# Optimization experiments

Measured on AMD Instinct MI355X. Metric: run time of the kernel, lower is better.

The kernel has to match this reference:

```python
import jax, jax.numpy as jnp
import numpy as np

L, N, EMB, H = 4, 50000, 128, 4
R, HID, LBL = 16, 64, 32
E = 625000


def setup_inputs() -> dict:
    key = jax.random.key(0)
    ks = jax.random.split(key, 10)
    s = 0.05
    return {
        "embedding": jax.random.normal(ks[0], (L, N, EMB), jnp.float32),
        "in_proj_w": jax.random.normal(ks[1], (3 * EMB, EMB), jnp.float32) * s,
        "in_proj_b": jnp.zeros((3 * EMB,), jnp.float32),
        "out_proj_w": jax.random.normal(ks[2], (EMB, EMB), jnp.float32) * s,
        "out_proj_b": jnp.zeros((EMB,), jnp.float32),
        "w1": jax.random.normal(ks[3], (R, EMB, HID), jnp.float32) * s,
        "root1": jax.random.normal(ks[4], (EMB, HID), jnp.float32) * s,
        "b1": jnp.zeros((HID,), jnp.float32),
        "w2": jax.random.normal(ks[5], (R, HID, LBL), jnp.float32) * s,
        "root2": jax.random.normal(ks[6], (HID, LBL), jnp.float32) * s,
        "b2": jnp.zeros((LBL,), jnp.float32),
        "edge_index": jax.random.randint(ks[7], (2, E), 0, N, dtype=jnp.int64),
        "edge_type": jax.random.randint(ks[8], (E,), 0, R, dtype=jnp.int64),
    }


def mha_self(x, wi, bi, wo, bo):
    # x: (L, N, EMB) -- torch nn.MultiheadAttention, batch_first=False, q=k=v=x
    Ls, Ns, Es = x.shape
    hd = Es // H
    qkv = x @ wi.T + bi                      # (L, N, 3E)
    q, k, v = jnp.split(qkv, 3, axis=-1)
    q = q.reshape(Ls, Ns, H, hd)
    k = k.reshape(Ls, Ns, H, hd)
    v = v.reshape(Ls, Ns, H, hd)
    scores = jnp.einsum('lnhd,mnhd->nhlm', q, k) / np.sqrt(hd).astype(np.float32)
    attn = jax.nn.softmax(scores, axis=-1)
    out = jnp.einsum('nhlm,mnhd->lnhd', attn, v).reshape(Ls, Ns, Es)
    return out @ wo.T + bo


def rgcn_layer(x, src, dst, etype, W, root, bias):
    # PyG RGCNConv (num_bases=None, aggr='mean'):
    # out[n] = x[n] @ root + bias + sum_r mean_{e: dst=n, type=r} x[src_e] @ W[r]
    Rr, fin, fout = W.shape
    seg = etype * N + dst                                   # (E,) combined (rel, dst)
    msg_sum = jax.ops.segment_sum(x[src], seg, num_segments=Rr * N)   # (R*N, fin)
    cnt = jax.ops.segment_sum(jnp.ones((src.shape[0],), x.dtype), seg,
                              num_segments=Rr * N)
    mean = (msg_sum / jnp.maximum(cnt, 1.0)[:, None]).reshape(Rr, N, fin)
    agg = jnp.einsum('rni,rio->no', mean, W)                # per-relation GEMM
    return agg + x @ root + bias


def reference(embedding, in_proj_w, in_proj_b, out_proj_w, out_proj_b,
              w1, root1, b1, w2, root2, b2, edge_index, edge_type):
    attn_out = mha_self(embedding, in_proj_w, in_proj_b, out_proj_w, out_proj_b)
    x = attn_out[0]                                         # (N, EMB)
    src, dst = edge_index[0], edge_index[1]
    x = jax.nn.relu(rgcn_layer(x, src, dst, edge_type, w1, root1, b1))
    x = rgcn_layer(x, src, dst, edge_type, w2, root2, b2)
    return jax.nn.softmax(x, axis=-1)
```

## Files before the change

kernel.cpp:

```cpp
#include <hip/hip_runtime.h>
#include <hip/hip_bf16.h>
#include <math.h>

#define NNODES 50000
#define NEDGE 625000
#define RREL 16
#define SCAN_NB 196

typedef __attribute__((ext_vector_type(8))) short short8;
typedef __attribute__((ext_vector_type(4))) float f32x4;

__device__ __forceinline__ float bfu(ushort u) {
  return __uint_as_float(((unsigned)u) << 16);
}
__device__ __forceinline__ ushort f2b(float f) {
  __hip_bfloat16 h = __float2bfloat16(f);
  return *(ushort*)&h;
}

__global__ __launch_bounds__(256) void mega_prep(
    const float* __restrict__ ipw, const float* __restrict__ opw,
    const float* __restrict__ w1, const float* __restrict__ root1,
    const float* __restrict__ w2, const float* __restrict__ root2,
    const float* __restrict__ opb,
    const int* __restrict__ dst, const int* __restrict__ et,
    __hip_bfloat16* __restrict__ BTqkv, __hip_bfloat16* __restrict__ BToutT,
    __hip_bfloat16* __restrict__ BT1, __hip_bfloat16* __restrict__ BT2,
    float* __restrict__ bias1, int* __restrict__ cnt) {
  int b = blockIdx.x, t = threadIdx.x;
  if (b < 944) {
    int i = b * 256 + t;
    if (i < 49152) {
      BTqkv[i] = __float2bfloat16(ipw[i]);
    } else if (i < 65536) {
      int j = i - 49152; int m = j / 128, c = j % 128;
      BToutT[j] = __float2bfloat16(opw[c * 128 + m]);
    } else if (i < 65536 + 139264) {
      int j = i - 65536; int c = j / 128, k = j % 128;
      float v;
      if (c < 64) v = root1[k * 64 + c];
      else { int r = (c - 64) >> 6, o = (c - 64) & 63; v = w1[r * 8192 + k * 64 + o]; }
      BT1[j] = __float2bfloat16(v);
    } else if (i < 65536 + 139264 + 34816) {
      int j = i - 65536 - 139264; int c = j / 64, k = j % 64;
      float v;
      if (c < 32) v = root2[k * 32 + c];
      else { int r = (c - 32) >> 5, o = (c - 32) & 31; v = w2[r * 2048 + k * 32 + o]; }
      BT2[j] = __float2bfloat16(v);
    }
  } else if (b < 949) {
    int j = (b - 944) * 256 + t;
    if (j < 1088) {
      float s = 0.f;
      if (j < 64) {
        for (int c = 0; c < 128; c++) s += opb[c] * root1[c * 64 + j];
      } else {
        int r = (j - 64) >> 6, o = (j - 64) & 63;
        for (int c = 0; c < 128; c++) s += opb[c] * w1[r * 8192 + c * 64 + o];
      }
      bias1[j] = s;
    }
  } else {
    int e = (b - 949) * 256 + t;
    if (e < NEDGE) atomicAdd(&cnt[et[e] * NNODES + dst[e]], 1);
  }
}

__global__ __launch_bounds__(256) void qkv_gemm(
    const float* __restrict__ A, const __hip_bfloat16* __restrict__ BT,
    const float* __restrict__ bias, __hip_bfloat16* __restrict__ C) {
  __shared__ ushort As[128 * 128];
  __shared__ ushort Cs[128 * 136];
  const int t = threadIdx.x;
  const long row0 = (long)blockIdx.x * 128;

  {
    float4 fa[16];
#pragma unroll
    for (int it = 0; it < 8; it++) {
      int c = t + it * 256;
      int r = c >> 4, cc = c & 15;
      long gm = row0 + r; if (gm > 199999) gm = 199999;
      const float* ap = A + gm * 128 + cc * 8;
      fa[2 * it]     = *(const float4*)ap;
      fa[2 * it + 1] = *(const float4*)(ap + 4);
    }
#pragma unroll
    for (int it = 0; it < 8; it++) {
      int c = t + it * 256;
      int r = c >> 4, cc = c & 15;
      int4 v = make_int4(0, 0, 0, 0);
      if (row0 + r < 200000) {
        float4 f0 = fa[2 * it], f1 = fa[2 * it + 1];
        v.x = (int)f2b(f0.x) | ((int)f2b(f0.y) << 16);
        v.y = (int)f2b(f0.z) | ((int)f2b(f0.w) << 16);
        v.z = (int)f2b(f1.x) | ((int)f2b(f1.y) << 16);
        v.w = (int)f2b(f1.z) | ((int)f2b(f1.w) << 16);
      }
      *(int4*)(As + r * 128 + ((cc ^ (r & 7)) * 8)) = v;
    }
  }
  __syncthreads();

  const int lane = t & 63, w = t >> 6;
  const int wr = (w >> 1) * 64, wc = (w & 1) * 64;
  const int lrow = lane & 15, lk = lane >> 4;
  const int nstrips = (row0 < NNODES) ? 3 : 2;

  for (int s = 0; s < nstrips; s++) {
    const int col0 = (s == 2) ? 0 : 128 + s * 128;
    const long Meff = (s == 2) ? NNODES : 200000;

    const ushort* bp[4];
#pragma unroll
    for (int j = 0; j < 4; j++)
      bp[j] = (const ushort*)BT + (long)(col0 + wc + j * 16 + lrow) * 128 + lk * 8;

    short8 bfr[4][4];
#pragma unroll
    for (int k0 = 0; k0 < 4; k0++)
#pragma unroll
      for (int j = 0; j < 4; j++)
        bfr[k0][j] = *(const short8*)(bp[j] + k0 * 32);

    f32x4 acc[4][4];
#pragma unroll
    for (int i = 0; i < 4; i++)
#pragma unroll
      for (int j = 0; j < 4; j++) acc[i][j] = (f32x4){0.f, 0.f, 0.f, 0.f};

#pragma unroll
    for (int k0 = 0; k0 < 4; k0++) {
      const int cb = k0 * 4 + lk;
      short8 af[4];
#pragma unroll
      for (int i = 0; i < 4; i++) {
        int ra = wr + i * 16 + lrow;
        af[i] = *(const short8*)(As + ra * 128 + ((cb ^ (ra & 7)) * 8));
      }
#pragma unroll
      for (int i = 0; i < 4; i++)
#pragma unroll
        for (int j = 0; j < 4; j++)
          acc[i][j] = __builtin_amdgcn_mfma_f32_16x16x32_bf16(af[i], bfr[k0][j], acc[i][j], 0, 0, 0);
    }

    __syncthreads();
#pragma unroll
    for (int j = 0; j < 4; j++) {
      int coll = wc + j * 16 + lrow;
      float bv = bias[col0 + coll];
#pragma unroll
      for (int i = 0; i < 4; i++) {
        int rbase = wr + i * 16 + lk * 4;
#pragma unroll
        for (int q = 0; q < 4; q++)
          Cs[(rbase + q) * 136 + coll] = f2b(acc[i][j][q] + bv);
      }
    }
    __syncthreads();
#pragma unroll
    for (int idx = t; idx < 128 * 16; idx += 256) {
      int r = idx >> 4, k = idx & 15;
      long gm = row0 + r;
      if (gm < Meff)
        *(int4*)((ushort*)C + gm * 384 + col0 + k * 8) = *(const int4*)(Cs + r * 136 + k * 8);
    }
  }
}

#define EPILOGUE_STORE(MEFF, NCOLS, LDC, BIASEXPR)                              \
  for (int p = 0; p < 2; p++) {                                                 \
    __syncthreads();                                                            \
    if ((w >> 1) == p) {                                                        \
      _Pragma("unroll")                                                         \
      for (int j = 0; j < 4; j++) {                                             \
        int coll = wc + j * 16 + lrow;                                          \
        float bv = (BIASEXPR);                                                  \
        _Pragma("unroll")                                                       \
        for (int i = 0; i < 4; i++) {                                           \
          int rloc = i * 16 + lk * 4;                                           \
          _Pragma("unroll")                                                     \
          for (int q = 0; q < 4; q++)                                           \
            Cs[(rloc + q) * 132 + coll] = f2b(acc[i][j][q] + bv);               \
        }                                                                       \
      }                                                                         \
    }                                                                           \
    __syncthreads();                                                            \
    _Pragma("unroll")                                                           \
    for (int idx = t; idx < 64 * 16; idx += 256) {                              \
      int r = idx >> 4, k = idx & 15;                                           \
      long gm = row0 + p * 64 + r;                                              \
      int col = col0 + k * 8;                                                   \
      if (gm < (MEFF) && col < (NCOLS))                                         \
        *(int4*)((ushort*)C + gm * (LDC) + col) = *(const int4*)(Cs + r * 132 + k * 8); \
    }                                                                           \
  }

template <int K>
__global__ __launch_bounds__(256) void gemm_strips(
    const __hip_bfloat16* __restrict__ Av, const __hip_bfloat16* __restrict__ BT,
    const float* __restrict__ bias, __hip_bfloat16* __restrict__ C,
    int M, int N, int ldc, int spg) {
  constexpr int CPR = K / 8;
  constexpr int NIT = 128 * CPR / 256;
  constexpr int NK0 = K / 32;
  __shared__ ushort As[128 * K];
  __shared__ ushort Cs[64 * 132];
  const int t = threadIdx.x;
  const long row0 = (long)blockIdx.x * 128;

  {
    int4 st[NIT];
#pragma unroll
    for (int it = 0; it < NIT; it++) {
      int c = t + it * 256;
      int r = c / CPR, cc = c % CPR;
      long gm = row0 + r; if (gm > M - 1) gm = M - 1;
      st[it] = *(const int4*)((const ushort*)Av + gm * K + cc * 8);
    }
#pragma unroll
    for (int it = 0; it < NIT; it++) {
      int c = t + it * 256;
      int r = c / CPR, cc = c % CPR;
      int4 v = (row0 + r < M) ? st[it] : make_int4(0, 0, 0, 0);
      *(int4*)(As + r * K + ((cc ^ (r & 7)) * 8)) = v;
    }
  }
  __syncthreads();

  const int lane = t & 63, w = t >> 6;
  const int wr = (w >> 1) * 64, wc = (w & 1) * 64;
  const int lrow = lane & 15, lk = lane >> 4;
  const int nstrips = (N + 127) / 128;
  const int sbeg = blockIdx.y * spg;
  const int send = min(sbeg + spg, nstrips);

  for (int s = sbeg; s < send; s++) {
    const int col0 = s * 128;

    const ushort* bp[4];
#pragma unroll
    for (int j = 0; j < 4; j++) {
      int gn = col0 + wc + j * 16 + lrow;
      if (gn > N - 1) gn = N - 1;
      bp[j] = (const ushort*)BT + (long)gn * K + lk * 8;
    }

    short8 bfr[NK0][4];
#pragma unroll
    for (int k0 = 0; k0 < NK0; k0++)
#pragma unroll
      for (int j = 0; j < 4; j++)
        bfr[k0][j] = *(const short8*)(bp[j] + k0 * 32);

    f32x4 acc[4][4];
#pragma unroll
    for (int i = 0; i < 4; i++)
#pragma unroll
      for (int j = 0; j < 4; j++) acc[i][j] = (f32x4){0.f, 0.f, 0.f, 0.f};

#pragma unroll
    for (int k0 = 0; k0 < NK0; k0++) {
      const int cb = k0 * 4 + lk;
      short8 af[4];
#pragma unroll
      for (int i = 0; i < 4; i++) {
        int ra = wr + i * 16 + lrow;
        af[i] = *(const short8*)(As + ra * K + ((cb ^ (ra & 7)) * 8));
      }
#pragma unroll
      for (int i = 0; i < 4; i++)
#pragma unroll
        for (int j = 0; j < 4; j++)
          acc[i][j] = __builtin_amdgcn_mfma_f32_16x16x32_bf16(af[i], bfr[k0][j], acc[i][j], 0, 0, 0);
    }

    EPILOGUE_STORE(M, N, ldc, bias ? bias[min(col0 + coll, N - 1)] : 0.f)
  }
}

__global__ __launch_bounds__(256) void attn_kernel(
    const __hip_bfloat16* __restrict__ qkv, __hip_bfloat16* __restrict__ o0) {
  int w = threadIdx.x >> 6, lane = threadIdx.x & 63;
  int nl = lane >> 4, cl = lane & 15;
  long n = (long)blockIdx.x * 16 + w * 4 + nl;
  const ushort* base = (const ushort*)qkv;
  int4 qv = *(const int4*)(base + n * 384 + cl * 8);
  int4 kq[4], vq[4];
#pragma unroll
  for (int m = 0; m < 4; m++) {
    const ushort* p = base + ((long)m * NNODES + n) * 384;
    kq[m] = *(const int4*)(p + 128 + cl * 8);
    vq[m] = *(const int4*)(p + 256 + cl * 8);
  }
  float qf[8];
  {
    const uint* qu = (const uint*)&qv;
#pragma unroll
    for (int x = 0; x < 4; x++) {
      qf[2 * x] = bfu(qu[x] & 0xffff);
      qf[2 * x + 1] = bfu(qu[x] >> 16);
    }
  }
  float s[4];
#pragma unroll
  for (int m = 0; m < 4; m++) {
    const uint* ku = (const uint*)&kq[m];
    float p = 0.f;
#pragma unroll
    for (int x = 0; x < 4; x++)
      p += qf[2 * x] * bfu(ku[x] & 0xffff) + qf[2 * x + 1] * bfu(ku[x] >> 16);
    p += __shfl_xor(p, 1);
    p += __shfl_xor(p, 2);
    s[m] = p * 0.17677669529663687f;
  }
  float mx = fmaxf(fmaxf(s[0], s[1]), fmaxf(s[2], s[3]));
  float e[4], sum = 0.f;
#pragma unroll
  for (int m = 0; m < 4; m++) { e[m] = __expf(s[m] - mx); sum += e[m]; }
  float inv = 1.0f / sum;
  float o[8] = {0.f, 0.f, 0.f, 0.f, 0.f, 0.f, 0.f, 0.f};
#pragma unroll
  for (int m = 0; m < 4; m++) {
    const uint* vu = (const uint*)&vq[m];
    float wgt = e[m] * inv;
#pragma unroll
    for (int x = 0; x < 4; x++) {
      o[2 * x]     += wgt * bfu(vu[x] & 0xffff);
      o[2 * x + 1] += wgt * bfu(vu[x] >> 16);
    }
  }
  int4 ov;
  uint* ou = (uint*)&ov;
#pragma unroll
  for (int x = 0; x < 4; x++)
    ou[x] = (uint)f2b(o[2 * x]) | ((uint)f2b(o[2 * x + 1]) << 16);
  *(int4*)((ushort*)o0 + n * 128 + cl * 8) = ov;
}

__global__ __launch_bounds__(256) void scan1(
    const int* __restrict__ cnt, int* __restrict__ off, int* __restrict__ part) {
  int t = threadIdx.x, b = blockIdx.x;
  int i = b * 256 + t;
  int v = 0;
  if (i < NNODES) {
#pragma unroll
    for (int r = 0; r < RREL; r++) v += cnt[r * NNODES + i];
  }
  __shared__ int sm[256];
  sm[t] = v;
  __syncthreads();
#pragma unroll
  for (int o = 1; o < 256; o <<= 1) {
    int x = (t >= o) ? sm[t - o] : 0;
    __syncthreads();
    sm[t] += x;
    __syncthreads();
  }
  if (i < NNODES) off[i] = sm[t] - v;
  if (t == 255) part[b] = sm[t];
}

__global__ __launch_bounds__(256) void scan2(int* __restrict__ part) {
  int t = threadIdx.x;
  int v = (t < SCAN_NB) ? part[t] : 0;
  __shared__ int sm[256];
  sm[t] = v;
  __syncthreads();
#pragma unroll
  for (int o = 1; o < 256; o <<= 1) {
    int x = (t >= o) ? sm[t - o] : 0;
    __syncthreads();
    sm[t] += x;
    __syncthreads();
  }
  if (t < SCAN_NB) part[t] = sm[t] - v;
}

__global__ __launch_bounds__(256) void scan3(int* __restrict__ off, const int* __restrict__ part) {
  int i = blockIdx.x * 256 + threadIdx.x;
  if (i < NNODES) off[i] += part[blockIdx.x];
  if (i == 0) off[NNODES] = NEDGE;
}

__global__ __launch_bounds__(256) void scatter_edges(
    const int* __restrict__ src, const int* __restrict__ dst, const int* __restrict__ et,
    const int* __restrict__ cnt, const int* __restrict__ off,
    int* __restrict__ fill, unsigned* __restrict__ sorted, float* __restrict__ scales) {
  int e = blockIdx.x * 256 + threadIdx.x;
  if (e >= NEDGE) return;
  int d = dst[e], r = et[e], s = src[e];
  int pos = off[d] + atomicAdd(&fill[d], 1);
  sorted[pos] = (unsigned)s | ((unsigned)r << 16);
  scales[pos] = 1.0f / (float)cnt[r * NNODES + d];
}

__global__ __launch_bounds__(256) void fused1(
    const int* __restrict__ off, const unsigned* __restrict__ sorted,
    const float* __restrict__ scales, const ushort* __restrict__ Y1,
    const float* __restrict__ b1, __hip_bfloat16* __restrict__ x1b) {
  int w = threadIdx.x >> 6, lane = threadIdx.x & 63;
  int d = blockIdx.x * 4 + w;
  int s0 = off[d], s1 = off[d + 1];
  float a[8];
  a[0] = bfu(Y1[(size_t)d * 1088 + lane]) + b1[lane];
#pragma unroll
  for (int j = 1; j < 8; j++) a[j] = 0.f;
  int i = s0;
  for (; i + 7 < s1; i += 8) {
    unsigned p[8];
    float c[8];
#pragma unroll
    for (int j = 0; j < 8; j++) { p[j] = sorted[i + j]; c[j] = scales[i + j]; }
#pragma unroll
    for (int j = 0; j < 8; j++)
      a[j] += bfu(Y1[(size_t)(p[j] & 0xFFFF) * 1088 + 64 + (p[j] >> 16) * 64 + lane]) * c[j];
  }
  for (; i < s1; i++) {
    unsigned p = sorted[i];
    a[0] += bfu(Y1[(size_t)(p & 0xFFFF) * 1088 + 64 + (p >> 16) * 64 + lane]) * scales[i];
  }
  float acc = ((a[0] + a[1]) + (a[2] + a[3])) + ((a[4] + a[5]) + (a[6] + a[7]));
  x1b[(size_t)d * 64 + lane] = __float2bfloat16(fmaxf(acc, 0.f));
}

__global__ __launch_bounds__(256) void fused2(
    const int* __restrict__ off, const unsigned* __restrict__ sorted,
    const float* __restrict__ scales, const ushort* __restrict__ Y2,
    const float* __restrict__ b2, float* __restrict__ out) {
  int w = threadIdx.x >> 6, lane = threadIdx.x & 63;
  int d = blockIdx.x * 4 + w;
  int j = lane & 31, half = lane >> 5;
  int s0 = off[d], s1 = off[d + 1];
  float a0 = 0.f, a1 = 0.f, a2 = 0.f, a3 = 0.f;
  int i = s0 + half;
  for (; i + 6 < s1; i += 8) {
    unsigned p0 = sorted[i], p1 = sorted[i + 2], p2 = sorted[i + 4], p3 = sorted[i + 6];
    float c0 = scales[i], c1 = scales[i + 2], c2 = scales[i + 4], c3 = scales[i + 6];
    a0 += bfu(Y2[(size_t)(p0 & 0xFFFF) * 544 + 32 + (p0 >> 16) * 32 + j]) * c0;
    a1 += bfu(Y2[(size_t)(p1 & 0xFFFF) * 544 + 32 + (p1 >> 16) * 32 + j]) * c1;
    a2 += bfu(Y2[(size_t)(p2 & 0xFFFF) * 544 + 32 + (p2 >> 16) * 32 + j]) * c2;
    a3 += bfu(Y2[(size_t)(p3 & 0xFFFF) * 544 + 32 + (p3 >> 16) * 32 + j]) * c3;
  }
  for (; i < s1; i += 2) {
    unsigned p = sorted[i];
    a0 += bfu(Y2[(size_t)(p & 0xFFFF) * 544 + 32 + (p >> 16) * 32 + j]) * scales[i];
  }
  float acc = (a0 + a1) + (a2 + a3);
  acc += __shfl_xor(acc, 32);
  float v = acc + bfu(Y2[(size_t)d * 544 + j]) + b2[j];
  float mx = v;
#pragma unroll
  for (int o = 16; o; o >>= 1) mx = fmaxf(mx, __shfl_xor(mx, o));
  float e = __expf(v - mx);
  float sum = e;
#pragma unroll
  for (int o = 16; o; o >>= 1) sum += __shfl_xor(sum, o);
  if (half == 0) out[(size_t)d * 32 + j] = e / sum;
}

extern "C" void kernel_launch(void* const* d_in, const int* in_sizes, int n_in,
                              void* d_out, int out_size, void* d_ws, size_t ws_size,
                              hipStream_t stream) {
  (void)in_sizes; (void)n_in; (void)out_size; (void)ws_size;
  const float* emb   = (const float*)d_in[0];
  const float* ipw   = (const float*)d_in[1];
  const float* ipb   = (const float*)d_in[2];
  const float* opw   = (const float*)d_in[3];
  const float* opb   = (const float*)d_in[4];
  const float* w1    = (const float*)d_in[5];
  const float* root1 = (const float*)d_in[6];
  const float* b1    = (const float*)d_in[7];
  const float* w2    = (const float*)d_in[8];
  const float* root2 = (const float*)d_in[9];
  const float* b2    = (const float*)d_in[10];
  const int*   eidx  = (const int*)d_in[11];
  const int*   etype = (const int*)d_in[12];
  const int* srcp = eidx;
  const int* dstp = eidx + NEDGE;

  unsigned char* ws = (unsigned char*)d_ws;
  size_t off_b = 0;
  auto alloc = [&](size_t bytes) {
    unsigned char* p = ws + off_b;
    off_b += (bytes + 255) & ~(size_t)255;
    return p;
  };

  unsigned char* R = alloc(153600000);
  __hip_bfloat16* qkv = (__hip_bfloat16*)R;
  __hip_bfloat16* Y1  = (__hip_bfloat16*)R;
  __hip_bfloat16* Y2  = (__hip_bfloat16*)R;
  __hip_bfloat16* o0  = (__hip_bfloat16*)alloc(12800000);
  __hip_bfloat16* x1b = (__hip_bfloat16*)alloc(6400000);
  int*            cnt = (int*)alloc(3200000);
  int*            offs = (int*)alloc((NNODES + 1) * 4);
  int*            fill = (int*)alloc(NNODES * 4);
  int*            part = (int*)alloc(SCAN_NB * 4);
  unsigned*       sorted = (unsigned*)alloc(NEDGE * 4);
  float*          scales = (float*)alloc(NEDGE * 4);
  __hip_bfloat16* BTqkv  = (__hip_bfloat16*)alloc(98304);
  __hip_bfloat16* BToutT = (__hip_bfloat16*)alloc(32768);
  __hip_bfloat16* BT1    = (__hip_bfloat16*)alloc(278528);
  __hip_bfloat16* BT2    = (__hip_bfloat16*)alloc(69632);
  __hip_bfloat16* BW     = (__hip_bfloat16*)alloc(278528);
  float*          bias1  = (float*)alloc(4352);

  hipMemsetAsync(cnt, 0, (size_t)RREL * NNODES * sizeof(int), stream);
  hipMemsetAsync(fill, 0, (size_t)NNODES * sizeof(int), stream);
  mega_prep<<<dim3(3391), dim3(256), 0, stream>>>(
      ipw, opw, w1, root1, w2, root2, opb, dstp, etype,
      BTqkv, BToutT, BT1, BT2, bias1, cnt);
  scan1<<<dim3(SCAN_NB), dim3(256), 0, stream>>>(cnt, offs, part);
  scan2<<<dim3(1), dim3(256), 0, stream>>>(part);
  scan3<<<dim3(SCAN_NB), dim3(256), 0, stream>>>(offs, part);
  scatter_edges<<<dim3((NEDGE + 255) / 256), dim3(256), 0, stream>>>(
      srcp, dstp, etype, cnt, offs, fill, sorted, scales);

  gemm_strips<128><<<dim3(9, 1), dim3(256), 0, stream>>>(
      BT1, BToutT, nullptr, BW, 1088, 128, 128, 1);

  qkv_gemm<<<dim3(1563), dim3(256), 0, stream>>>(emb, BTqkv, ipb, qkv);

  attn_kernel<<<dim3(3125), dim3(256), 0, stream>>>(qkv, o0);

  gemm_strips<128><<<dim3(391, 3), dim3(256), 0, stream>>>(
      o0, BW, bias1, Y1, NNODES, 1088, 1088, 3);

  fused1<<<dim3(NNODES / 4), dim3(256), 0, stream>>>(
      offs, sorted, scales, (const ushort*)Y1, b1, x1b);

  gemm_strips<64><<<dim3(391, 2), dim3(256), 0, stream>>>(
      x1b, BT2, nullptr, Y2, NNODES, 544, 544, 3);

  fused2<<<dim3(NNODES / 4), dim3(256), 0, stream>>>(
      offs, sorted, scales, (const ushort*)Y2, b2, (float*)d_out);
}
```

Baseline: 320.2 us.

## Pre-convert embedding to bf16 and use direct global-to-LDS loads in GEMMs

Moves the fp32-to-bf16 conversion of the embedding into the prep kernel, writing a separate bf16 buffer. qkv_gemm then loads it directly. Both qkv_gemm and gemm_strips replace the register-staged A-tile load with global_load_lds 16-byte transfers, keeping the XOR swizzle. This frees registers and instructions in the GEMMs, at the cost of an extra full read and write pass over the embedding. Out-of-range rows are no longer zeroed but clamped to a duplicate row.

```diff
diff --git a/kernel.cpp b/kernel.cpp
--- a/kernel.cpp
+++ b/kernel.cpp
@@ -16,6 +16,11 @@
 __device__ __forceinline__ ushort f2b(float f) {
   __hip_bfloat16 h = __float2bfloat16(f);
   return *(ushort*)&h;
+}
+__device__ __forceinline__ void gl_lds16(const ushort* g, ushort* l) {
+  __builtin_amdgcn_global_load_lds(
+      (__attribute__((address_space(1))) void*)(void*)g,
+      (__attribute__((address_space(3))) void*)(void*)l, 16, 0, 0);
 }
 
 __global__ __launch_bounds__(256) void mega_prep(
@@ -24,9 +29,11 @@
     const float* __restrict__ w2, const float* __restrict__ root2,
     const float* __restrict__ opb,
     const int* __restrict__ dst, const int* __restrict__ et,
+    const float* __restrict__ emb,
     __hip_bfloat16* __restrict__ BTqkv, __hip_bfloat16* __restrict__ BToutT,
     __hip_bfloat16* __restrict__ BT1, __hip_bfloat16* __restrict__ BT2,
-    float* __restrict__ bias1, int* __restrict__ cnt) {
+    float* __restrict__ bias1, int* __restrict__ cnt,
+    __hip_bfloat16* __restrict__ embb) {
   int b = blockIdx.x, t = threadIdx.x;
   if (b < 944) {
     int i = b * 256 + t;
@@ -60,49 +67,43 @@
       }
       bias1[j] = s;
     }
-  } else {
+  } else if (b < 3391) {
     int e = (b - 949) * 256 + t;
     if (e < NEDGE) atomicAdd(&cnt[et[e] * NNODES + dst[e]], 1);
+  } else {
+    long i = (long)(b - 3391) * 2048 + t * 8;
+    float4 a = *(const float4*)(emb + i);
+    float4 c = *(const float4*)(emb + i + 4);
+    int4 v;
+    v.x = (int)f2b(a.x) | ((int)f2b(a.y) << 16);
+    v.y = (int)f2b(a.z) | ((int)f2b(a.w) << 16);
+    v.z = (int)f2b(c.x) | ((int)f2b(c.y) << 16);
+    v.w = (int)f2b(c.z) | ((int)f2b(c.w) << 16);
+    *(int4*)((ushort*)embb + i) = v;
   }
 }
 
 __global__ __launch_bounds__(256) void qkv_gemm(
-    const float* __restrict__ A, const __hip_bfloat16* __restrict__ BT,
+    const __hip_bfloat16* __restrict__ Av, const __hip_bfloat16* __restrict__ BT,
     const float* __restrict__ bias, __hip_bfloat16* __restrict__ C) {
   __shared__ ushort As[128 * 128];
   __shared__ ushort Cs[128 * 136];
   const int t = threadIdx.x;
+  const int lane = t & 63, w = t >> 6;
   const long row0 = (long)blockIdx.x * 128;
-
-  {
-    float4 fa[16];
-#pragma unroll
-    for (int it = 0; it < 8; it++) {
-      int c = t + it * 256;
-      int r = c >> 4, cc = c & 15;
-      long gm = row0 + r; if (gm > 199999) gm = 199999;
-      const float* ap = A + gm * 128 + cc * 8;
-      fa[2 * it]     = *(const float4*)ap;
-      fa[2 * it + 1] = *(const float4*)(ap + 4);
-    }
-#pragma unroll
-    for (int it = 0; it < 8; it++) {
-      int c = t + it * 256;
-      int r = c >> 4, cc = c & 15;
-      int4 v = make_int4(0, 0, 0, 0);
-      if (row0 + r < 200000) {
-        float4 f0 = fa[2 * it], f1 = fa[2 * it + 1];
-        v.x = (int)f2b(f0.x) | ((int)f2b(f0.y) << 16);
-        v.y = (int)f2b(f0.z) | ((int)f2b(f0.w) << 16);
-        v.z = (int)f2b(f1.x) | ((int)f2b(f1.y) << 16);
-        v.w = (int)f2b(f1.z) | ((int)f2b(f1.w) << 16);
-      }
-      *(int4*)(As + r * 128 + ((cc ^ (r & 7)) * 8)) = v;
-    }
+  const ushort* A = (const ushort*)Av;
+
+#pragma unroll
+  for (int i = 0; i < 8; i++) {
+    int cb0 = w * 512 + i * 64;
+    int chunk = cb0 + lane;
+    int r = chunk >> 4, cs = chunk & 15;
+    long gm = row0 + r; if (gm > 199999) gm = 199999;
+    int cc = cs ^ (r & 7);
+    gl_lds16(A + gm * 128 + cc * 8, As + cb0 * 8);
   }
   __syncthreads();
 
-  const int lane = t & 63, w = t >> 6;
   const int wr = (w >> 1) * 64, wc = (w & 1) * 64;
   const int lrow = lane & 15, lk = lane >> 4;
   const int nstrips = (row0 < NNODES) ? 3 : 2;
@@ -203,33 +204,27 @@
     const float* __restrict__ bias, __hip_bfloat16* __restrict__ C,
     int M, int N, int ldc, int spg) {
   constexpr int CPR = K / 8;
-  constexpr int NIT = 128 * CPR / 256;
+  constexpr int TOTCH = 128 * CPR;
+  constexpr int NI = TOTCH / 256;
   constexpr int NK0 = K / 32;
   __shared__ ushort As[128 * K];
   __shared__ ushort Cs[64 * 132];
   const int t = threadIdx.x;
+  const int lane = t & 63, w = t >> 6;
   const long row0 = (long)blockIdx.x * 128;
-
-  {
-    int4 st[NIT];
-#pragma unroll
-    for (int it = 0; it < NIT; it++) {
-      int c = t + it * 256;
-      int r = c / CPR, cc = c % CPR;
-      long gm = row0 + r; if (gm > M - 1) gm = M - 1;
-      st[it] = *(const int4*)((const ushort*)Av + gm * K + cc * 8);
-    }
-#pragma unroll
-    for (int it = 0; it < NIT; it++) {
-      int c = t + it * 256;
-      int r = c / CPR, cc = c % CPR;
-      int4 v = (row0 + r < M) ? st[it] : make_int4(0, 0, 0, 0);
-      *(int4*)(As + r * K + ((cc ^ (r & 7)) * 8)) = v;
-    }
+  const ushort* A = (const ushort*)Av;
+
+#pragma unroll
+  for (int i = 0; i < NI; i++) {
+    int cb0 = w * (TOTCH / 4) + i * 64;
+    int chunk = cb0 + lane;
+    int r = chunk / CPR, cs = chunk % CPR;
+    long gm = row0 + r; if (gm > M - 1) gm = M - 1;
+    int cc = cs ^ (r & 7);
+    gl_lds16(A + gm * K + cc * 8, As + cb0 * 8);
   }
   __syncthreads();
 
-  const int lane = t & 63, w = t >> 6;
   const int wr = (w >> 1) * 64, wc = (w & 1) * 64;
   const int lrow = lane & 15, lk = lane >> 4;
   const int nstrips = (N + 127) / 128;
@@ -492,6 +487,7 @@
   __hip_bfloat16* qkv = (__hip_bfloat16*)R;
   __hip_bfloat16* Y1  = (__hip_bfloat16*)R;
   __hip_bfloat16* Y2  = (__hip_bfloat16*)R;
+  __hip_bfloat16* embb = (__hip_bfloat16*)alloc(51200000);
   __hip_bfloat16* o0  = (__hip_bfloat16*)alloc(12800000);
   __hip_bfloat16* x1b = (__hip_bfloat16*)alloc(6400000);
   int*            cnt = (int*)alloc(3200000);
@@ -509,9 +505,9 @@
 
   hipMemsetAsync(cnt, 0, (size_t)RREL * NNODES * sizeof(int), stream);
   hipMemsetAsync(fill, 0, (size_t)NNODES * sizeof(int), stream);
-  mega_prep<<<dim3(3391), dim3(256), 0, stream>>>(
-      ipw, opw, w1, root1, w2, root2, opb, dstp, etype,
-      BTqkv, BToutT, BT1, BT2, bias1, cnt);
+  mega_prep<<<dim3(15891), dim3(256), 0, stream>>>(
+      ipw, opw, w1, root1, w2, root2, opb, dstp, etype, emb,
+      BTqkv, BToutT, BT1, BT2, bias1, cnt, embb);
   scan1<<<dim3(SCAN_NB), dim3(256), 0, stream>>>(cnt, offs, part);
   scan2<<<dim3(1), dim3(256), 0, stream>>>(part);
   scan3<<<dim3(SCAN_NB), dim3(256), 0, stream>>>(offs, part);
@@ -521,7 +517,7 @@
   gemm_strips<128><<<dim3(9, 1), dim3(256), 0, stream>>>(
       BT1, BToutT, nullptr, BW, 1088, 128, 128, 1);
 
-  qkv_gemm<<<dim3(1563), dim3(256), 0, stream>>>(emb, BTqkv, ipb, qkv);
+  qkv_gemm<<<dim3(1563), dim3(256), 0, stream>>>(embb, BTqkv, ipb, qkv);
 
   attn_kernel<<<dim3(3125), dim3(256), 0, stream>>>(qkv, o0);
 
```

Result: slower. 333.8 us (+4.3%).
